# Optimization experiments

Hardware: AMD Instinct MI355X
Metric: run time of the kernel (lower is better)

Reference implementation:

```python
import jax, jax.numpy as jnp
import numpy as np

N_VARS = 2048
BATCH = 1024


def encode_input(pos):
    # pos: [n_vars, batch] -> [2*n_vars + 2, batch]
    # row 0 = 0, row 1 = 1, even rows >=2 = pos, odd rows >=3 = 1 - pos
    n = pos.shape[0]
    out = jnp.zeros((2 * n + 2,) + pos.shape[1:], dtype=pos.dtype)
    out = out.at[1].set(1.0)
    out = out.at[2::2].set(pos)
    out = out.at[3::2].set(1.0 - pos)
    return out


def setup_inputs() -> dict:
    key = jax.random.key(0)
    k0, k1, k2, k3, k4 = jax.random.split(key, 5)
    x = jax.random.uniform(k0, (N_VARS, BATCH), dtype=jnp.float32)
    idx0 = jax.random.randint(k1, (32768, 2), 0, 2 * N_VARS + 2, dtype=jnp.int32)
    idx1 = jax.random.randint(k2, (16384, 2), 0, 32768, dtype=jnp.int32)
    idx2 = jax.random.randint(k3, (8192, 2), 0, 16384, dtype=jnp.int32)
    idx3 = jax.random.randint(k4, (4096, 2), 0, 8192, dtype=jnp.int32)
    return {"x": x, "idx0": idx0, "idx1": idx1, "idx2": idx2, "idx3": idx3}


def reference(x, idx0, idx1, idx2, idx3):
    h = encode_input(x)                  # [2*n_vars+2, B]
    h = h[idx0].prod(axis=1)             # ProductLayer: [32768, B]
    h = h[idx1].sum(axis=1)              # SumLayer:     [16384, B]
    h = h[idx2].prod(axis=1)             # ProductLayer: [8192, B]
    h = h[idx3].sum(axis=1)              # SumLayer:     [4096, B]
    return h
```

## Files before the change

kernel.cpp:

```cpp
#include <hip/hip_runtime.h>
#include <hip/hip_fp16.h>

#define BATCH  1024
#define NVARS  2048
#define N_OUT  4096

#define W32BYTES (NVARS * 64)
#define NW32     (BATCH / 32)

typedef float f32x4 __attribute__((ext_vector_type(4)));

__device__ __forceinline__ __half2 u2h2(unsigned u) {
    union { unsigned u; __half2 h; } c; c.u = u; return c.h;
}
__device__ __forceinline__ unsigned h22u(__half2 h) {
    union { unsigned u; __half2 h; } c; c.h = h; return c.u;
}
__device__ __forceinline__ void sel2sc(unsigned sel, unsigned& s, unsigned& c) {
    c = (sel & 1u) ? 0x3C003C00u : 0u;
    s = (sel == 2u) ? 0x3C003C00u : (sel == 3u) ? 0xBC00BC00u : 0u;
}

__global__ __launch_bounds__(256) void prep_kernel(
    const float* __restrict__ x,
    const int2* __restrict__ idx0,
    const int2* __restrict__ idx1,
    const int2* __restrict__ idx2,
    const int2* __restrict__ idx3,
    unsigned* __restrict__ T,
    char* __restrict__ xh2)
{
    __shared__ char tile[64 * 272];

    const int bid = blockIdx.x;
    const int tid = threadIdx.x;
    const int rt  = bid >> 3;
    const int ct  = bid & 7;
    const int r0  = rt * 64;

    if (bid < 16) {
        const int i = bid * 256 + tid;
        int2 p3 = idx3[i];
        int n = 0;
        #pragma unroll
        for (int t = 0; t < 2; ++t) {
            int2 p2 = idx2[t ? p3.y : p3.x];
            #pragma unroll
            for (int u = 0; u < 2; ++u) {
                int2 p1 = idx1[u ? p2.y : p2.x];
                #pragma unroll
                for (int v = 0; v < 2; ++v) {
                    int2 p0 = idx0[v ? p1.y : p1.x];
                    unsigned w = 0;
                    #pragma unroll
                    for (int e = 0; e < 2; ++e) {
                        int k = e ? p0.y : p0.x;
                        unsigned code;
                        if (k < 2) code = (unsigned)k << 11;
                        else       code = ((2u + (k & 1)) << 11) | ((unsigned)(k - 2) >> 1);
                        w |= code << (16 * e);
                    }
                    T[(size_t)i * 8 + n] = w;
                    ++n;
                }
            }
        }
    }

    {
        const int r_l = tid >> 5;
        const int c4  = tid & 31;
        #pragma unroll
        for (int q = 0; q < 8; ++q) {
            const int rr = q * 8 + r_l;
            float4 v = ((const float4*)x)[(size_t)(r0 + rr) * 256 + ct * 32 + c4];
            unsigned h0 = h22u(__floats2half2_rn(v.x, v.y));
            unsigned h1 = h22u(__floats2half2_rn(v.z, v.w));
            unsigned* p = (unsigned*)(tile + rr * 272 + c4 * 8);
            p[0] = h0; p[1] = h1;
        }
    }
    __syncthreads();

    {
        const int wl = tid & 3;
        const int r2 = tid >> 2;
        #pragma unroll
        for (int g = 0; g < 4; ++g) {
            uint4 v = *(const uint4*)(tile + r2 * 272 + g * 64 + wl * 16);
            const int w32 = ct * 4 + g;
            *(uint4*)(xh2 + (size_t)w32 * W32BYTES + (r0 + r2) * 64 + wl * 16) = v;
        }
    }
}

__global__ __launch_bounds__(512) void knowledge_main(
    const char* __restrict__ xh2,
    const uint4* __restrict__ T4,
    float* __restrict__ out)
{
    __shared__ char lds[131072];

    const int bx   = blockIdx.x;
    const int tid  = threadIdx.x;
    const int xcd  = bx & 7;
    const int slot = bx >> 3;
    const int w    = xcd * 4 + (slot & 3);
    const int chunk= slot >> 2;

    {
        const char* src = xh2 + (size_t)w * W32BYTES;
        #pragma unroll
        for (int it = 0; it < 16; ++it) {
            const int u = it * 512 + tid;
            *(uint4*)(lds + u * 16) = *(const uint4*)(src + u * 16);
        }
    }
    __syncthreads();

    const int cg  = tid & 3;
    const int ol  = tid >> 2;
    const int cgb = cg * 16;

    #pragma unroll 1
    for (int pass = 0; pass < 4; ++pass) {
        const int o = chunk * 512 + pass * 128 + ol;
        uint4 t0 = T4[(size_t)o * 2];
        uint4 t1 = T4[(size_t)o * 2 + 1];
        const unsigned tw[8] = {t0.x, t0.y, t0.z, t0.w, t1.x, t1.y, t1.z, t1.w};

        float accf[8];
        #pragma unroll
        for (int k = 0; k < 8; ++k) accf[k] = 0.f;

        #pragma unroll
        for (int a3 = 0; a3 < 2; ++a3) {
            __half2 prod2[4];
            #pragma unroll
            for (int a2 = 0; a2 < 2; ++a2) {
                __half2 sum1[4];
                #pragma unroll
                for (int a1 = 0; a1 < 2; ++a1) {
                    const int m = a3 * 4 + a2 * 2 + a1;
                    const unsigned wv = tw[m];
                    uint4 A = *(const uint4*)(lds + ((wv & 0x7FFu) << 6) + cgb);
                    uint4 B = *(const uint4*)(lds + (((wv >> 16) & 0x7FFu) << 6) + cgb);
                    unsigned sa, ca, sb, cb;
                    sel2sc((wv >> 11) & 3u, sa, ca);
                    sel2sc((wv >> 27) & 3u, sb, cb);
                    const unsigned aw[4] = {A.x, A.y, A.z, A.w};
                    const unsigned bw[4] = {B.x, B.y, B.z, B.w};
                    #pragma unroll
                    for (int k = 0; k < 4; ++k) {
                        __half2 va = __hfma2(u2h2(aw[k]), u2h2(sa), u2h2(ca));
                        __half2 vb = __hfma2(u2h2(bw[k]), u2h2(sb), u2h2(cb));
                        __half2 pr = __hmul2(va, vb);
                        sum1[k] = (a1 == 0) ? pr : __hadd2(sum1[k], pr);
                    }
                }
                #pragma unroll
                for (int k = 0; k < 4; ++k)
                    prod2[k] = (a2 == 0) ? sum1[k] : __hmul2(prod2[k], sum1[k]);
            }
            #pragma unroll
            for (int k = 0; k < 4; ++k) {
                float2 pf = __half22float2(prod2[k]);
                accf[2 * k]     += pf.x;
                accf[2 * k + 1] += pf.y;
            }
        }

        float* dst = out + (size_t)o * BATCH + w * 32 + cg * 8;
        f32x4 o0 = {accf[0], accf[1], accf[2], accf[3]};
        f32x4 o1 = {accf[4], accf[5], accf[6], accf[7]};
        __builtin_nontemporal_store(o0, reinterpret_cast<f32x4*>(dst));
        __builtin_nontemporal_store(o1, reinterpret_cast<f32x4*>(dst) + 1);
    }
}

__device__ __forceinline__ float Hval(int k, const float* __restrict__ x, int b) {
    if (k < 2) return (float)k;
    float v = x[((k - 2) >> 1) * BATCH + b];
    return (k & 1) ? 1.0f - v : v;
}

__global__ __launch_bounds__(256) void knowledge_fused_kernel(
    const float* __restrict__ x,
    const int2* __restrict__ idx0,
    const int2* __restrict__ idx1,
    const int2* __restrict__ idx2,
    const int2* __restrict__ idx3,
    float* __restrict__ out)
{
    const int i = blockIdx.x;
    const int b = blockIdx.y * blockDim.x + threadIdx.x;
    const int2 p3 = idx3[i];
    float acc3 = 0.0f;
    #pragma unroll
    for (int t = 0; t < 2; ++t) {
        const int2 p2 = idx2[t ? p3.y : p3.x];
        float prod2 = 1.0f;
        #pragma unroll
        for (int u = 0; u < 2; ++u) {
            const int2 p1 = idx1[u ? p2.y : p2.x];
            float sum1 = 0.0f;
            #pragma unroll
            for (int v = 0; v < 2; ++v) {
                const int2 p0 = idx0[v ? p1.y : p1.x];
                sum1 += Hval(p0.x, x, b) * Hval(p0.y, x, b);
            }
            prod2 *= sum1;
        }
        acc3 += prod2;
    }
    out[(size_t)i * BATCH + b] = acc3;
}

extern "C" void kernel_launch(void* const* d_in, const int* in_sizes, int n_in,
                              void* d_out, int out_size, void* d_ws, size_t ws_size,
                              hipStream_t stream) {
    const float* x    = (const float*)d_in[0];
    const int2*  idx0 = (const int2*)d_in[1];
    const int2*  idx1 = (const int2*)d_in[2];
    const int2*  idx2 = (const int2*)d_in[3];
    const int2*  idx3 = (const int2*)d_in[4];
    float* out = (float*)d_out;

    const size_t t_bytes   = (size_t)N_OUT * 8 * sizeof(unsigned);
    const size_t xh2_bytes = (size_t)NW32 * W32BYTES;
    if (ws_size >= t_bytes + xh2_bytes) {
        unsigned* T   = (unsigned*)d_ws;
        char*     xh2 = (char*)d_ws + t_bytes;
        prep_kernel<<<256, 256, 0, stream>>>(x, idx0, idx1, idx2, idx3, T, xh2);
        knowledge_main<<<256, 512, 0, stream>>>(xh2, (const uint4*)T, out);
    } else {
        dim3 grid(N_OUT, BATCH / 256);
        knowledge_fused_kernel<<<grid, 256, 0, stream>>>(x, idx0, idx1, idx2, idx3, out);
    }
}
```

Before: 19.18 us.

## Fuse prep and main kernels into one launch with per-block index walk

Merges the separate prep kernel, which converted x to fp16 column slabs and resolved the index tree into a table, into the main kernel. Each 1024-thread block now loads its 32-column fp16 slab straight from x into LDS and resolves its own 512 outputs' index codes into LDS. This removes one kernel launch and the workspace round-trip. In exchange each x slab is read and converted redundantly by several blocks, the strided float4 loads from x are less coalesced, and 1024-thread blocks with 144KB of LDS may limit occupancy.

```diff
diff --git a/kernel.cpp b/kernel.cpp
--- a/kernel.cpp
+++ b/kernel.cpp
@@ -4,9 +4,6 @@
 #define BATCH  1024
 #define NVARS  2048
 #define N_OUT  4096
-
-#define W32BYTES (NVARS * 64)
-#define NW32     (BATCH / 32)
 
 typedef float f32x4 __attribute__((ext_vector_type(4)));
 
@@ -21,25 +18,40 @@
     s = (sel == 2u) ? 0x3C003C00u : (sel == 3u) ? 0xBC00BC00u : 0u;
 }
 
-__global__ __launch_bounds__(256) void prep_kernel(
+__global__ __launch_bounds__(1024) void knowledge_all(
     const float* __restrict__ x,
     const int2* __restrict__ idx0,
     const int2* __restrict__ idx1,
     const int2* __restrict__ idx2,
     const int2* __restrict__ idx3,
-    unsigned* __restrict__ T,
-    char* __restrict__ xh2)
+    float* __restrict__ out)
 {
-    __shared__ char tile[64 * 272];
+    __shared__ char     lds[131072];
+    __shared__ unsigned Tl[512 * 8];
 
-    const int bid = blockIdx.x;
-    const int tid = threadIdx.x;
-    const int rt  = bid >> 3;
-    const int ct  = bid & 7;
-    const int r0  = rt * 64;
+    const int bx    = blockIdx.x;
+    const int tid   = threadIdx.x;
+    const int xcd   = bx & 7;
+    const int slot  = bx >> 3;
+    const int w     = xcd * 4 + (slot & 3);
+    const int chunk = slot >> 2;
 
-    if (bid < 16) {
-        const int i = bid * 256 + tid;
+    {
+        const float* xw = x + w * 32;
+        #pragma unroll
+        for (int it = 0; it < 16; ++it) {
+            const int u = it * 1024 + tid;
+            const int r = u >> 3, p = u & 7;
+            float4 v = *(const float4*)(xw + (size_t)r * BATCH + p * 4);
+            uint2 d;
+            d.x = h22u(__floats2half2_rn(v.x, v.y));
+            d.y = h22u(__floats2half2_rn(v.z, v.w));
+            *(uint2*)(lds + r * 64 + p * 8) = d;
+        }
+    }
+
+    if (tid < 512) {
+        const int i = chunk * 512 + tid;
         int2 p3 = idx3[i];
         int n = 0;
         #pragma unroll
@@ -51,69 +63,19 @@
                 #pragma unroll
                 for (int v = 0; v < 2; ++v) {
                     int2 p0 = idx0[v ? p1.y : p1.x];
-                    unsigned w = 0;
+                    unsigned wc = 0;
                     #pragma unroll
                     for (int e = 0; e < 2; ++e) {
                         int k = e ? p0.y : p0.x;
                         unsigned code;
                         if (k < 2) code = (unsigned)k << 11;
                         else       code = ((2u + (k & 1)) << 11) | ((unsigned)(k - 2) >> 1);
-                        w |= code << (16 * e);
+                        wc |= code << (16 * e);
                     }
-                    T[(size_t)i * 8 + n] = w;
+                    Tl[tid * 8 + n] = wc;
                     ++n;
                 }
             }
-        }
-    }
-
-    {
-        const int r_l = tid >> 5;
-        const int c4  = tid & 31;
-        #pragma unroll
-        for (int q = 0; q < 8; ++q) {
-            const int rr = q * 8 + r_l;
-            float4 v = ((const float4*)x)[(size_t)(r0 + rr) * 256 + ct * 32 + c4];
-            unsigned h0 = h22u(__floats2half2_rn(v.x, v.y));
-            unsigned h1 = h22u(__floats2half2_rn(v.z, v.w));
-            unsigned* p = (unsigned*)(tile + rr * 272 + c4 * 8);
-            p[0] = h0; p[1] = h1;
-        }
-    }
-    __syncthreads();
-
-    {
-        const int wl = tid & 3;
-        const int r2 = tid >> 2;
-        #pragma unroll
-        for (int g = 0; g < 4; ++g) {
-            uint4 v = *(const uint4*)(tile + r2 * 272 + g * 64 + wl * 16);
-            const int w32 = ct * 4 + g;
-            *(uint4*)(xh2 + (size_t)w32 * W32BYTES + (r0 + r2) * 64 + wl * 16) = v;
-        }
-    }
-}
-
-__global__ __launch_bounds__(512) void knowledge_main(
-    const char* __restrict__ xh2,
-    const uint4* __restrict__ T4,
-    float* __restrict__ out)
-{
-    __shared__ char lds[131072];
-
-    const int bx   = blockIdx.x;
-    const int tid  = threadIdx.x;
-    const int xcd  = bx & 7;
-    const int slot = bx >> 3;
-    const int w    = xcd * 4 + (slot & 3);
-    const int chunk= slot >> 2;
-
-    {
-        const char* src = xh2 + (size_t)w * W32BYTES;
-        #pragma unroll
-        for (int it = 0; it < 16; ++it) {
-            const int u = it * 512 + tid;
-            *(uint4*)(lds + u * 16) = *(const uint4*)(src + u * 16);
         }
     }
     __syncthreads();
@@ -123,11 +85,11 @@
     const int cgb = cg * 16;
 
     #pragma unroll 1
-    for (int pass = 0; pass < 4; ++pass) {
-        const int o = chunk * 512 + pass * 128 + ol;
-        uint4 t0 = T4[(size_t)o * 2];
-        uint4 t1 = T4[(size_t)o * 2 + 1];
-        const unsigned tw[8] = {t0.x, t0.y, t0.z, t0.w, t1.x, t1.y, t1.z, t1.w};
+    for (int pass = 0; pass < 2; ++pass) {
+        const int oloc = pass * 256 + ol;
+        const unsigned* tp = &Tl[oloc * 8];
+        const unsigned tw[8] = {tp[0], tp[1], tp[2], tp[3],
+                                tp[4], tp[5], tp[6], tp[7]};
 
         float accf[8];
         #pragma unroll
@@ -170,50 +132,13 @@
             }
         }
 
+        const int o = chunk * 512 + oloc;
         float* dst = out + (size_t)o * BATCH + w * 32 + cg * 8;
         f32x4 o0 = {accf[0], accf[1], accf[2], accf[3]};
         f32x4 o1 = {accf[4], accf[5], accf[6], accf[7]};
         __builtin_nontemporal_store(o0, reinterpret_cast<f32x4*>(dst));
         __builtin_nontemporal_store(o1, reinterpret_cast<f32x4*>(dst) + 1);
     }
-}
-
-__device__ __forceinline__ float Hval(int k, const float* __restrict__ x, int b) {
-    if (k < 2) return (float)k;
-    float v = x[((k - 2) >> 1) * BATCH + b];
-    return (k & 1) ? 1.0f - v : v;
-}
-
-__global__ __launch_bounds__(256) void knowledge_fused_kernel(
-    const float* __restrict__ x,
-    const int2* __restrict__ idx0,
-    const int2* __restrict__ idx1,
-    const int2* __restrict__ idx2,
-    const int2* __restrict__ idx3,
-    float* __restrict__ out)
-{
-    const int i = blockIdx.x;
-    const int b = blockIdx.y * blockDim.x + threadIdx.x;
-    const int2 p3 = idx3[i];
-    float acc3 = 0.0f;
-    #pragma unroll
-    for (int t = 0; t < 2; ++t) {
-        const int2 p2 = idx2[t ? p3.y : p3.x];
-        float prod2 = 1.0f;
-        #pragma unroll
-        for (int u = 0; u < 2; ++u) {
-            const int2 p1 = idx1[u ? p2.y : p2.x];
-            float sum1 = 0.0f;
-            #pragma unroll
-            for (int v = 0; v < 2; ++v) {
-                const int2 p0 = idx0[v ? p1.y : p1.x];
-                sum1 += Hval(p0.x, x, b) * Hval(p0.y, x, b);
-            }
-            prod2 *= sum1;
-        }
-        acc3 += prod2;
-    }
-    out[(size_t)i * BATCH + b] = acc3;
 }
 
 extern "C" void kernel_launch(void* const* d_in, const int* in_sizes, int n_in,
@@ -226,15 +151,5 @@
     const int2*  idx3 = (const int2*)d_in[4];
     float* out = (float*)d_out;
 
-    const size_t t_bytes   = (size_t)N_OUT * 8 * sizeof(unsigned);
-    const size_t xh2_bytes = (size_t)NW32 * W32BYTES;
-    if (ws_size >= t_bytes + xh2_bytes) {
-        unsigned* T   = (unsigned*)d_ws;
-        char*     xh2 = (char*)d_ws + t_bytes;
-        prep_kernel<<<256, 256, 0, stream>>>(x, idx0, idx1, idx2, idx3, T, xh2);
-        knowledge_main<<<256, 512, 0, stream>>>(xh2, (const uint4*)T, out);
-    } else {
-        dim3 grid(N_OUT, BATCH / 256);
-        knowledge_fused_kernel<<<grid, 256, 0, stream>>>(x, idx0, idx1, idx2, idx3, out);
-    }
+    knowledge_all<<<256, 1024, 0, stream>>>(x, idx0, idx1, idx2, idx3, out);
 }
```

Measured after the change: 20.64 us. 7.6% more time.

## Software-pipeline LDS gathers and prefetch index tables across passes

Applied to the files above, without the earlier changes.

Unrolls the four passes of the main kernel into a double-buffered pipeline: the first two passes' index words are loaded before the LDS fill, and the LDS gathers for the next pass are issued before the math of the current one. This hides the global latency of the index loads and the LDS gather latency behind the arithmetic. It also switches the prep kernel's workspace writes to nontemporal stores. The cost is much higher register pressure (two sets of 16 uint4 gathers live at once), which at 512 threads per block could cause spills.

```diff
diff --git a/kernel.cpp b/kernel.cpp
--- a/kernel.cpp
+++ b/kernel.cpp
@@ -9,6 +9,7 @@
 #define NW32     (BATCH / 32)
 
 typedef float f32x4 __attribute__((ext_vector_type(4)));
+typedef unsigned u32x4 __attribute__((ext_vector_type(4)));
 
 __device__ __forceinline__ __half2 u2h2(unsigned u) {
     union { unsigned u; __half2 h; } c; c.u = u; return c.h;
@@ -60,7 +61,7 @@
                         else       code = ((2u + (k & 1)) << 11) | ((unsigned)(k - 2) >> 1);
                         w |= code << (16 * e);
                     }
-                    T[(size_t)i * 8 + n] = w;
+                    __builtin_nontemporal_store(w, &T[(size_t)i * 8 + n]);
                     ++n;
                 }
             }
@@ -87,12 +88,70 @@
         const int r2 = tid >> 2;
         #pragma unroll
         for (int g = 0; g < 4; ++g) {
-            uint4 v = *(const uint4*)(tile + r2 * 272 + g * 64 + wl * 16);
+            u32x4 v = *reinterpret_cast<const u32x4*>(tile + r2 * 272 + g * 64 + wl * 16);
             const int w32 = ct * 4 + g;
-            *(uint4*)(xh2 + (size_t)w32 * W32BYTES + (r0 + r2) * 64 + wl * 16) = v;
-        }
-    }
-}
+            __builtin_nontemporal_store(
+                v, reinterpret_cast<u32x4*>(
+                       xh2 + (size_t)w32 * W32BYTES + (r0 + r2) * 64 + wl * 16));
+        }
+    }
+}
+
+#define ISSUE16(TW, AA, T0, T1)                                               \
+    do {                                                                      \
+        TW[0]=(T0).x; TW[1]=(T0).y; TW[2]=(T0).z; TW[3]=(T0).w;               \
+        TW[4]=(T1).x; TW[5]=(T1).y; TW[6]=(T1).z; TW[7]=(T1).w;               \
+        _Pragma("unroll")                                                     \
+        for (int m = 0; m < 8; ++m) {                                         \
+            AA[2*m]   = *(const uint4*)(lds + ((TW[m] & 0x7FFu) << 6) + cgb); \
+            AA[2*m+1] = *(const uint4*)(lds + (((TW[m] >> 16) & 0x7FFu) << 6) + cgb); \
+        }                                                                     \
+    } while (0)
+
+#define MATHSTORE(TW, AA, OO)                                                 \
+    do {                                                                      \
+        float accf[8];                                                        \
+        _Pragma("unroll") for (int k = 0; k < 8; ++k) accf[k] = 0.f;          \
+        _Pragma("unroll")                                                     \
+        for (int a3 = 0; a3 < 2; ++a3) {                                      \
+            __half2 prod2[4];                                                 \
+            _Pragma("unroll")                                                 \
+            for (int a2 = 0; a2 < 2; ++a2) {                                  \
+                __half2 sum1[4];                                              \
+                _Pragma("unroll")                                             \
+                for (int a1 = 0; a1 < 2; ++a1) {                              \
+                    const int m = a3 * 4 + a2 * 2 + a1;                       \
+                    const unsigned wv = TW[m];                                \
+                    unsigned sa, ca, sb, cb;                                  \
+                    sel2sc((wv >> 11) & 3u, sa, ca);                          \
+                    sel2sc((wv >> 27) & 3u, sb, cb);                          \
+                    const unsigned aw[4] = {AA[2*m].x, AA[2*m].y, AA[2*m].z, AA[2*m].w}; \
+                    const unsigned bw[4] = {AA[2*m+1].x, AA[2*m+1].y, AA[2*m+1].z, AA[2*m+1].w}; \
+                    _Pragma("unroll")                                         \
+                    for (int k = 0; k < 4; ++k) {                             \
+                        __half2 va = __hfma2(u2h2(aw[k]), u2h2(sa), u2h2(ca)); \
+                        __half2 vb = __hfma2(u2h2(bw[k]), u2h2(sb), u2h2(cb)); \
+                        __half2 pr = __hmul2(va, vb);                         \
+                        sum1[k] = (a1 == 0) ? pr : __hadd2(sum1[k], pr);      \
+                    }                                                         \
+                }                                                             \
+                _Pragma("unroll")                                             \
+                for (int k = 0; k < 4; ++k)                                   \
+                    prod2[k] = (a2 == 0) ? sum1[k] : __hmul2(prod2[k], sum1[k]); \
+            }                                                                 \
+            _Pragma("unroll")                                                 \
+            for (int k = 0; k < 4; ++k) {                                     \
+                float2 pf = __half22float2(prod2[k]);                         \
+                accf[2*k]     += pf.x;                                        \
+                accf[2*k + 1] += pf.y;                                        \
+            }                                                                 \
+        }                                                                     \
+        float* dst = out + (size_t)(OO) * BATCH + w * 32 + cg * 8;            \
+        f32x4 o0 = {accf[0], accf[1], accf[2], accf[3]};                      \
+        f32x4 o1 = {accf[4], accf[5], accf[6], accf[7]};                      \
+        __builtin_nontemporal_store(o0, reinterpret_cast<f32x4*>(dst));       \
+        __builtin_nontemporal_store(o1, reinterpret_cast<f32x4*>(dst) + 1);   \
+    } while (0)
 
 __global__ __launch_bounds__(512) void knowledge_main(
     const char* __restrict__ xh2,
@@ -101,12 +160,22 @@
 {
     __shared__ char lds[131072];
 
-    const int bx   = blockIdx.x;
-    const int tid  = threadIdx.x;
-    const int xcd  = bx & 7;
-    const int slot = bx >> 3;
-    const int w    = xcd * 4 + (slot & 3);
-    const int chunk= slot >> 2;
+    const int bx    = blockIdx.x;
+    const int tid   = threadIdx.x;
+    const int xcd   = bx & 7;
+    const int slot  = bx >> 3;
+    const int w     = xcd * 4 + (slot & 3);
+    const int chunk = slot >> 2;
+
+    const int cg  = tid & 3;
+    const int ol  = tid >> 2;
+    const int cgb = cg * 16;
+    const int ob  = chunk * 512 + ol;
+
+    uint4 Ta0 = T4[(size_t)ob * 2];
+    uint4 Tb0 = T4[(size_t)ob * 2 + 1];
+    uint4 Ta1 = T4[(size_t)(ob + 128) * 2];
+    uint4 Tb1 = T4[(size_t)(ob + 128) * 2 + 1];
 
     {
         const char* src = xh2 + (size_t)w * W32BYTES;
@@ -118,64 +187,25 @@
     }
     __syncthreads();
 
-    const int cg  = tid & 3;
-    const int ol  = tid >> 2;
-    const int cgb = cg * 16;
-
-    #pragma unroll 1
-    for (int pass = 0; pass < 4; ++pass) {
-        const int o = chunk * 512 + pass * 128 + ol;
-        uint4 t0 = T4[(size_t)o * 2];
-        uint4 t1 = T4[(size_t)o * 2 + 1];
-        const unsigned tw[8] = {t0.x, t0.y, t0.z, t0.w, t1.x, t1.y, t1.z, t1.w};
-
-        float accf[8];
-        #pragma unroll
-        for (int k = 0; k < 8; ++k) accf[k] = 0.f;
-
-        #pragma unroll
-        for (int a3 = 0; a3 < 2; ++a3) {
-            __half2 prod2[4];
-            #pragma unroll
-            for (int a2 = 0; a2 < 2; ++a2) {
-                __half2 sum1[4];
-                #pragma unroll
-                for (int a1 = 0; a1 < 2; ++a1) {
-                    const int m = a3 * 4 + a2 * 2 + a1;
-                    const unsigned wv = tw[m];
-                    uint4 A = *(const uint4*)(lds + ((wv & 0x7FFu) << 6) + cgb);
-                    uint4 B = *(const uint4*)(lds + (((wv >> 16) & 0x7FFu) << 6) + cgb);
-                    unsigned sa, ca, sb, cb;
-                    sel2sc((wv >> 11) & 3u, sa, ca);
-                    sel2sc((wv >> 27) & 3u, sb, cb);
-                    const unsigned aw[4] = {A.x, A.y, A.z, A.w};
-                    const unsigned bw[4] = {B.x, B.y, B.z, B.w};
-                    #pragma unroll
-                    for (int k = 0; k < 4; ++k) {
-                        __half2 va = __hfma2(u2h2(aw[k]), u2h2(sa), u2h2(ca));
-                        __half2 vb = __hfma2(u2h2(bw[k]), u2h2(sb), u2h2(cb));
-                        __half2 pr = __hmul2(va, vb);
-                        sum1[k] = (a1 == 0) ? pr : __hadd2(sum1[k], pr);
-                    }
-                }
-                #pragma unroll
-                for (int k = 0; k < 4; ++k)
-                    prod2[k] = (a2 == 0) ? sum1[k] : __hmul2(prod2[k], sum1[k]);
-            }
-            #pragma unroll
-            for (int k = 0; k < 4; ++k) {
-                float2 pf = __half22float2(prod2[k]);
-                accf[2 * k]     += pf.x;
-                accf[2 * k + 1] += pf.y;
-            }
-        }
-
-        float* dst = out + (size_t)o * BATCH + w * 32 + cg * 8;
-        f32x4 o0 = {accf[0], accf[1], accf[2], accf[3]};
-        f32x4 o1 = {accf[4], accf[5], accf[6], accf[7]};
-        __builtin_nontemporal_store(o0, reinterpret_cast<f32x4*>(dst));
-        __builtin_nontemporal_store(o1, reinterpret_cast<f32x4*>(dst) + 1);
-    }
+    unsigned TWa[8], TWb[8];
+    uint4 Aa[16], Ab[16];
+
+    ISSUE16(TWa, Aa, Ta0, Tb0);
+
+    ISSUE16(TWb, Ab, Ta1, Tb1);
+    Ta0 = T4[(size_t)(ob + 256) * 2];
+    Tb0 = T4[(size_t)(ob + 256) * 2 + 1];
+    MATHSTORE(TWa, Aa, ob);
+
+    ISSUE16(TWa, Aa, Ta0, Tb0);
+    Ta1 = T4[(size_t)(ob + 384) * 2];
+    Tb1 = T4[(size_t)(ob + 384) * 2 + 1];
+    MATHSTORE(TWb, Ab, ob + 128);
+
+    ISSUE16(TWb, Ab, Ta1, Tb1);
+    MATHSTORE(TWa, Aa, ob + 256);
+
+    MATHSTORE(TWb, Ab, ob + 384);
 }
 
 __device__ __forceinline__ float Hval(int k, const float* __restrict__ x, int b) {
```

Result: slower. 20.26 us (+5.6%).
